# Kernel optimization log

Measured on AMD Instinct MI355X. Metric: run time of the kernel, lower is better.

## Reference

```python
import jax, jax.numpy as jnp
import numpy as np

B, S, H = 4, 1024, 256      # batch, num_spans, hidden
R = 65536                   # num_relations
FFN = int(2 * H * 1.5)      # 768


def setup_inputs() -> dict:
    key = jax.random.key(0)
    k1, k2, k3, k4 = jax.random.split(key, 4)
    span_reps = jax.random.normal(k1, (B, S, H), dtype=jnp.float32)
    rel_ids = jax.random.randint(k2, (B, R, 2), 0, S, dtype=jnp.int64)
    W1 = jax.random.normal(k3, (2 * H, FFN), dtype=jnp.float32) * (1.0 / np.sqrt(2 * H))
    b1 = jnp.zeros((FFN,), dtype=jnp.float32)
    W2 = jax.random.normal(k4, (FFN, H), dtype=jnp.float32) * (1.0 / np.sqrt(FFN))
    b2 = jnp.zeros((H,), dtype=jnp.float32)
    return {"span_reps": span_reps, "rel_ids": rel_ids, "W1": W1, "b1": b1, "W2": W2, "b2": b2}


def reference(span_reps, rel_ids, W1, b1, W2, b2):
    # gather head/tail span reps: (B, R, H) each
    head = jnp.take_along_axis(span_reps, rel_ids[..., 0:1], axis=1)  # via batched gather
    tail = jnp.take_along_axis(span_reps, rel_ids[..., 1:2], axis=1)
    rel = jnp.concatenate([head, tail], axis=-1)  # (B, R, 2H)
    # FFN projection: Linear -> ReLU -> (dropout: identity at eval) -> Linear
    h = jax.nn.relu(jnp.einsum('brk,kf->brf', rel, W1) + b1)
    out = jnp.einsum('brf,fh->brh', h, W2) + b2  # (B, R, H)
    return out
```

## Files before the change

### kernel.cpp

```cpp
#include <hip/hip_runtime.h>

#define NB 4
#define NS 1024
#define NH 256
#define NR 65536
#define NF 768
#define NK 512

typedef __attribute__((ext_vector_type(8))) short bf16x8;
typedef __attribute__((ext_vector_type(4))) float f32x4;

static __device__ __forceinline__ unsigned short f2bf(float f) {
  unsigned int u = __builtin_bit_cast(unsigned int, f);
  u += 0x7FFFu + ((u >> 16) & 1u);
  return (unsigned short)(u >> 16);
}

#define BARRIER()                                            \
  do {                                                       \
    asm volatile("s_waitcnt lgkmcnt(0)" ::: "memory");       \
    __builtin_amdgcn_s_barrier();                            \
    asm volatile("" ::: "memory");                           \
  } while (0)

__global__ void detect_idw(const int* __restrict__ ids, int* __restrict__ flag) {
  __shared__ int anynz;
  if (threadIdx.x == 0) anynz = 0;
  __syncthreads();
  int acc = 0;
  for (int i = threadIdx.x; i < 8192; i += 256) acc |= ids[2 * i + 1];
  if (acc != 0) atomicOr(&anynz, 1);
  __syncthreads();
  if (threadIdx.x == 0) flag[0] = (anynz == 0) ? 1 : 0;
}

__global__ void prep_w1(const float* __restrict__ w1, unsigned short* __restrict__ w1f) {
  int t = blockIdx.x * 256 + threadIdx.x;
  int l = t & 63;
  int kk = (t >> 6) & 15;
  int half = (t >> 10) & 1;
  int w = (t >> 11) & 3;
  int c = t >> 13;
  int row = c * 128 + w * 32 + half * 16 + (l & 15);
  int k0 = kk * 32 + (l >> 4) * 8;
  uint4 pk;
  unsigned short v[8];
#pragma unroll
  for (int j = 0; j < 8; ++j) v[j] = f2bf(w1[(size_t)(k0 + j) * NF + row]);
  pk.x = v[0] | ((unsigned)v[1] << 16);
  pk.y = v[2] | ((unsigned)v[3] << 16);
  pk.z = v[4] | ((unsigned)v[5] << 16);
  pk.w = v[6] | ((unsigned)v[7] << 16);
  *(uint4*)(w1f + (size_t)t * 8) = pk;
}

__global__ void prep_w2(const float* __restrict__ w2, unsigned short* __restrict__ w2f) {
  int t = blockIdx.x * 256 + threadIdx.x;
  int l = t & 63;
  int kq = (t >> 6) & 3;
  int rest = t >> 8;
  int c = rest % 6;
  int wn = rest / 6;
  int nj = wn & 3;
  int w = wn >> 2;
  int row = w * 64 + nj * 16 + (l & 15);
  int k = c * 128 + kq * 32 + (l >> 4) * 8;
  uint4 pk;
  unsigned short v[8];
#pragma unroll
  for (int j = 0; j < 8; ++j) v[j] = f2bf(w2[(size_t)(k + j) * NH + row]);
  pk.x = v[0] | ((unsigned)v[1] << 16);
  pk.y = v[2] | ((unsigned)v[3] << 16);
  pk.z = v[4] | ((unsigned)v[5] << 16);
  pk.w = v[6] | ((unsigned)v[7] << 16);
  *(uint4*)(w2f + (size_t)t * 8) = pk;
}

__global__ __launch_bounds__(256, 2)
void fused_relffn(const float* __restrict__ span, const int* __restrict__ ids,
                  const float* __restrict__ b1, const float* __restrict__ b2,
                  const unsigned short* __restrict__ w1f,
                  const unsigned short* __restrict__ w2f,
                  const int* __restrict__ flagp, float* __restrict__ out) {
  __shared__ __align__(16) unsigned short As[64 * 512];
  __shared__ __align__(16) unsigned short Hs[64 * 128];

  const int tid = threadIdx.x;
  const int blk = blockIdx.x;
  const int bb = blk >> 10;
  const int r0 = (blk & 1023) << 6;
  const int lane = tid & 63;
  const int w = tid >> 6;
  const int l15 = lane & 15;
  const int lq = lane >> 4;
  const int is64 = flagp[0];

  const unsigned short* w1base = w1f + w * 16384 + lane * 8;
  const unsigned short* w2base = w2f + w * 49152 + lane * 8;

  bf16x8 wf[4][2];
#pragma unroll
  for (int s = 0; s < 4; ++s) {
    wf[s][0] = *(const bf16x8*)(w1base + s * 512);
    wf[s][1] = *(const bf16x8*)(w1base + 8192 + s * 512);
  }

  {
    const long pair0 = ((long)bb * NR + r0) * 2;
#pragma unroll
    for (int j = 0; j < 16; ++j) {
      int g = tid + j * 256;
      int row = g >> 6;
      int kc = g & 63;
      long pidx = pair0 + row * 2 + (kc >> 5);
      int id = is64 ? ids[pidx * 2] : ids[pidx];
      const float* src = span + ((size_t)bb * NS + id) * NH + (kc & 31) * 8;
      float4 v0 = *(const float4*)src;
      float4 v1 = *(const float4*)(src + 4);
      uint4 pk;
      pk.x = f2bf(v0.x) | ((unsigned)f2bf(v0.y) << 16);
      pk.y = f2bf(v0.z) | ((unsigned)f2bf(v0.w) << 16);
      pk.z = f2bf(v1.x) | ((unsigned)f2bf(v1.y) << 16);
      pk.w = f2bf(v1.z) | ((unsigned)f2bf(v1.w) << 16);
      int idx = row * 512 + ((kc * 8) ^ ((row & 7) << 3));
      *(uint4*)&As[idx] = pk;
    }
  }
  BARRIER();

  f32x4 acc2[4][4];
#pragma unroll
  for (int mi = 0; mi < 4; ++mi)
#pragma unroll
    for (int nj = 0; nj < 4; ++nj) {
      f32x4 z = {0.f, 0.f, 0.f, 0.f};
      acc2[mi][nj] = z;
    }

  for (int c = 0; c < 6; ++c) {
    const unsigned short* w1p = w1base + c * 65536;
    f32x4 acc1[4][2];
#pragma unroll
    for (int mi = 0; mi < 4; ++mi)
#pragma unroll
      for (int ni = 0; ni < 2; ++ni) {
        f32x4 z = {0.f, 0.f, 0.f, 0.f};
        acc1[mi][ni] = z;
      }
#pragma unroll
    for (int kk = 0; kk < 16; ++kk) {
      const int s = kk & 3;
      bf16x8 cw0 = wf[s][0];
      bf16x8 cw1 = wf[s][1];
      if (kk < 12) {
        wf[s][0] = *(const bf16x8*)(w1p + (kk + 4) * 512);
        wf[s][1] = *(const bf16x8*)(w1p + 8192 + (kk + 4) * 512);
      }
      bf16x8 af[4];
#pragma unroll
      for (int mi = 0; mi < 4; ++mi) {
        int row = mi * 16 + l15;
        int kidx = kk * 32 + lq * 8;
        af[mi] = *(const bf16x8*)&As[row * 512 + (kidx ^ ((row & 7) << 3))];
      }
#pragma unroll
      for (int mi = 0; mi < 4; ++mi) {
        acc1[mi][0] = __builtin_amdgcn_mfma_f32_16x16x32_bf16(cw0, af[mi], acc1[mi][0], 0, 0, 0);
        acc1[mi][1] = __builtin_amdgcn_mfma_f32_16x16x32_bf16(cw1, af[mi], acc1[mi][1], 0, 0, 0);
      }
    }
    if (c < 5) {
      const unsigned short* np = w1base + (c + 1) * 65536;
#pragma unroll
      for (int s = 0; s < 4; ++s) {
        wf[s][0] = *(const bf16x8*)(np + s * 512);
        wf[s][1] = *(const bf16x8*)(np + 8192 + s * 512);
      }
    }
    BARRIER();
#pragma unroll
    for (int ni = 0; ni < 2; ++ni) {
      int n0 = c * 128 + w * 32 + ni * 16 + lq * 4;
      float4 bv = *(const float4*)(b1 + n0);
#pragma unroll
      for (int mi = 0; mi < 4; ++mi) {
        f32x4 a = acc1[mi][ni];
        float x0 = fmaxf(a[0] + bv.x, 0.0f);
        float x1 = fmaxf(a[1] + bv.y, 0.0f);
        float x2 = fmaxf(a[2] + bv.z, 0.0f);
        float x3 = fmaxf(a[3] + bv.w, 0.0f);
        int m = mi * 16 + l15;
        int nl0 = w * 32 + ni * 16 + lq * 4;
        uint2 pk;
        pk.x = f2bf(x0) | ((unsigned)f2bf(x1) << 16);
        pk.y = f2bf(x2) | ((unsigned)f2bf(x3) << 16);
        *(uint2*)&Hs[m * 128 + (nl0 ^ ((m & 7) << 3))] = pk;
      }
    }
    BARRIER();
    const unsigned short* w2p = w2base + c * 2048;
#pragma unroll
    for (int kq = 0; kq < 4; ++kq) {
      bf16x8 vf[4];
#pragma unroll
      for (int nj = 0; nj < 4; ++nj)
        vf[nj] = *(const bf16x8*)(w2p + nj * 12288 + kq * 512);
      bf16x8 hf[4];
#pragma unroll
      for (int mi = 0; mi < 4; ++mi) {
        int row = mi * 16 + l15;
        int kidx = kq * 32 + lq * 8;
        hf[mi] = *(const bf16x8*)&Hs[row * 128 + (kidx ^ ((row & 7) << 3))];
      }
#pragma unroll
      for (int mi = 0; mi < 4; ++mi)
#pragma unroll
        for (int nj = 0; nj < 4; ++nj)
          acc2[mi][nj] = __builtin_amdgcn_mfma_f32_16x16x32_bf16(vf[nj], hf[mi], acc2[mi][nj], 0, 0, 0);
    }
  }

#pragma unroll
  for (int nj = 0; nj < 4; ++nj) {
    int n0 = w * 64 + nj * 16 + lq * 4;
    float4 bv = *(const float4*)(b2 + n0);
#pragma unroll
    for (int mi = 0; mi < 4; ++mi) {
      int m = mi * 16 + l15;
      f32x4 a = acc2[mi][nj];
      float4 o;
      o.x = a[0] + bv.x; o.y = a[1] + bv.y; o.z = a[2] + bv.z; o.w = a[3] + bv.w;
      *(float4*)(out + ((size_t)bb * NR + r0 + m) * NH + n0) = o;
    }
  }
}

extern "C" void kernel_launch(void* const* d_in, const int* in_sizes, int n_in,
                              void* d_out, int out_size, void* d_ws, size_t ws_size,
                              hipStream_t stream) {
  const float* span = (const float*)d_in[0];
  const int* ids = (const int*)d_in[1];
  const float* W1 = (const float*)d_in[2];
  const float* b1 = (const float*)d_in[3];
  const float* W2 = (const float*)d_in[4];
  const float* b2 = (const float*)d_in[5];
  float* out = (float*)d_out;

  char* ws = (char*)d_ws;
  int* flag = (int*)ws;
  unsigned short* w1f = (unsigned short*)(ws + 64);
  unsigned short* w2f = (unsigned short*)(ws + 64 + NF * NK * 2);

  detect_idw<<<1, 256, 0, stream>>>(ids, flag);
  prep_w1<<<192, 256, 0, stream>>>(W1, w1f);
  prep_w2<<<96, 256, 0, stream>>>(W2, w2f);
  fused_relffn<<<4096, 256, 0, stream>>>(span, ids, b1, b2, w1f, w2f, flag, out);
}
```

Before: 347.2 us.

## Merge prep kernels, pair FFN chunks, double-buffer A fragments, use packed bf16 convert

Merges the three prep kernels into one launch to cut launch overhead. Batches the index loads before the span gathers so more memory requests are in flight. Uses the hardware packed bf16 conversion instruction in place of manual rounding. Restructures the first GEMM to compute two 128-wide FFN chunks per pass, sharing each A fragment across both and double-buffering LDS fragment loads. It also adds s_setprio around the MFMA blocks. Doubling the live accumulators raises register pressure, which may cost occupancy under the 2-block launch bound.

```diff
diff --git a/kernel.cpp b/kernel.cpp
--- a/kernel.cpp
+++ b/kernel.cpp
@@ -16,6 +16,12 @@
   return (unsigned short)(u >> 16);
 }
 
+static __device__ __forceinline__ unsigned cvt_pk(float a, float b) {
+  unsigned r;
+  asm("v_cvt_pk_bf16_f32 %0, %1, %2" : "=v"(r) : "v"(a), "v"(b));
+  return r;
+}
+
 #define BARRIER()                                            \
   do {                                                       \
     asm volatile("s_waitcnt lgkmcnt(0)" ::: "memory");       \
@@ -23,57 +29,60 @@
     asm volatile("" ::: "memory");                           \
   } while (0)
 
-__global__ void detect_idw(const int* __restrict__ ids, int* __restrict__ flag) {
-  __shared__ int anynz;
-  if (threadIdx.x == 0) anynz = 0;
-  __syncthreads();
-  int acc = 0;
-  for (int i = threadIdx.x; i < 8192; i += 256) acc |= ids[2 * i + 1];
-  if (acc != 0) atomicOr(&anynz, 1);
-  __syncthreads();
-  if (threadIdx.x == 0) flag[0] = (anynz == 0) ? 1 : 0;
-}
-
-__global__ void prep_w1(const float* __restrict__ w1, unsigned short* __restrict__ w1f) {
-  int t = blockIdx.x * 256 + threadIdx.x;
-  int l = t & 63;
-  int kk = (t >> 6) & 15;
-  int half = (t >> 10) & 1;
-  int w = (t >> 11) & 3;
-  int c = t >> 13;
-  int row = c * 128 + w * 32 + half * 16 + (l & 15);
-  int k0 = kk * 32 + (l >> 4) * 8;
-  uint4 pk;
-  unsigned short v[8];
-#pragma unroll
-  for (int j = 0; j < 8; ++j) v[j] = f2bf(w1[(size_t)(k0 + j) * NF + row]);
-  pk.x = v[0] | ((unsigned)v[1] << 16);
-  pk.y = v[2] | ((unsigned)v[3] << 16);
-  pk.z = v[4] | ((unsigned)v[5] << 16);
-  pk.w = v[6] | ((unsigned)v[7] << 16);
-  *(uint4*)(w1f + (size_t)t * 8) = pk;
-}
-
-__global__ void prep_w2(const float* __restrict__ w2, unsigned short* __restrict__ w2f) {
-  int t = blockIdx.x * 256 + threadIdx.x;
-  int l = t & 63;
-  int kq = (t >> 6) & 3;
-  int rest = t >> 8;
-  int c = rest % 6;
-  int wn = rest / 6;
-  int nj = wn & 3;
-  int w = wn >> 2;
-  int row = w * 64 + nj * 16 + (l & 15);
-  int k = c * 128 + kq * 32 + (l >> 4) * 8;
-  uint4 pk;
-  unsigned short v[8];
-#pragma unroll
-  for (int j = 0; j < 8; ++j) v[j] = f2bf(w2[(size_t)(k + j) * NH + row]);
-  pk.x = v[0] | ((unsigned)v[1] << 16);
-  pk.y = v[2] | ((unsigned)v[3] << 16);
-  pk.z = v[4] | ((unsigned)v[5] << 16);
-  pk.w = v[6] | ((unsigned)v[7] << 16);
-  *(uint4*)(w2f + (size_t)t * 8) = pk;
+__global__ void prep_all(const float* __restrict__ w1, const float* __restrict__ w2,
+                         const int* __restrict__ ids,
+                         unsigned short* __restrict__ w1f,
+                         unsigned short* __restrict__ w2f,
+                         int* __restrict__ flag) {
+  int bid = blockIdx.x;
+  if (bid < 192) {
+    int t = bid * 256 + threadIdx.x;
+    int l = t & 63;
+    int kk = (t >> 6) & 15;
+    int half = (t >> 10) & 1;
+    int w = (t >> 11) & 3;
+    int c = t >> 13;
+    int row = c * 128 + w * 32 + half * 16 + (l & 15);
+    int k0 = kk * 32 + (l >> 4) * 8;
+    uint4 pk;
+    unsigned short v[8];
+#pragma unroll
+    for (int j = 0; j < 8; ++j) v[j] = f2bf(w1[(size_t)(k0 + j) * NF + row]);
+    pk.x = v[0] | ((unsigned)v[1] << 16);
+    pk.y = v[2] | ((unsigned)v[3] << 16);
+    pk.z = v[4] | ((unsigned)v[5] << 16);
+    pk.w = v[6] | ((unsigned)v[7] << 16);
+    *(uint4*)(w1f + (size_t)t * 8) = pk;
+  } else if (bid < 288) {
+    int t = (bid - 192) * 256 + threadIdx.x;
+    int l = t & 63;
+    int kq = (t >> 6) & 3;
+    int rest = t >> 8;
+    int c = rest % 6;
+    int wn = rest / 6;
+    int nj = wn & 3;
+    int w = wn >> 2;
+    int row = w * 64 + nj * 16 + (l & 15);
+    int k = c * 128 + kq * 32 + (l >> 4) * 8;
+    uint4 pk;
+    unsigned short v[8];
+#pragma unroll
+    for (int j = 0; j < 8; ++j) v[j] = f2bf(w2[(size_t)(k + j) * NH + row]);
+    pk.x = v[0] | ((unsigned)v[1] << 16);
+    pk.y = v[2] | ((unsigned)v[3] << 16);
+    pk.z = v[4] | ((unsigned)v[5] << 16);
+    pk.w = v[6] | ((unsigned)v[7] << 16);
+    *(uint4*)(w2f + (size_t)t * 8) = pk;
+  } else {
+    __shared__ int anynz;
+    if (threadIdx.x == 0) anynz = 0;
+    __syncthreads();
+    int acc = 0;
+    for (int i = threadIdx.x; i < 8192; i += 256) acc |= ids[2 * i + 1];
+    if (acc != 0) atomicOr(&anynz, 1);
+    __syncthreads();
+    if (threadIdx.x == 0) flag[0] = (anynz == 0) ? 1 : 0;
+  }
 }
 
 __global__ __launch_bounds__(256, 2)
@@ -98,30 +107,30 @@
   const unsigned short* w1base = w1f + w * 16384 + lane * 8;
   const unsigned short* w2base = w2f + w * 49152 + lane * 8;
 
-  bf16x8 wf[4][2];
-#pragma unroll
-  for (int s = 0; s < 4; ++s) {
-    wf[s][0] = *(const bf16x8*)(w1base + s * 512);
-    wf[s][1] = *(const bf16x8*)(w1base + 8192 + s * 512);
-  }
-
   {
     const long pair0 = ((long)bb * NR + r0) * 2;
+    int idv[16];
 #pragma unroll
     for (int j = 0; j < 16; ++j) {
       int g = tid + j * 256;
       int row = g >> 6;
       int kc = g & 63;
       long pidx = pair0 + row * 2 + (kc >> 5);
-      int id = is64 ? ids[pidx * 2] : ids[pidx];
-      const float* src = span + ((size_t)bb * NS + id) * NH + (kc & 31) * 8;
+      idv[j] = is64 ? ids[pidx * 2] : ids[pidx];
+    }
+#pragma unroll
+    for (int j = 0; j < 16; ++j) {
+      int g = tid + j * 256;
+      int row = g >> 6;
+      int kc = g & 63;
+      const float* src = span + ((size_t)bb * NS + idv[j]) * NH + (kc & 31) * 8;
       float4 v0 = *(const float4*)src;
       float4 v1 = *(const float4*)(src + 4);
       uint4 pk;
-      pk.x = f2bf(v0.x) | ((unsigned)f2bf(v0.y) << 16);
-      pk.y = f2bf(v0.z) | ((unsigned)f2bf(v0.w) << 16);
-      pk.z = f2bf(v1.x) | ((unsigned)f2bf(v1.y) << 16);
-      pk.w = f2bf(v1.z) | ((unsigned)f2bf(v1.w) << 16);
+      pk.x = cvt_pk(v0.x, v0.y);
+      pk.y = cvt_pk(v0.z, v0.w);
+      pk.z = cvt_pk(v1.x, v1.y);
+      pk.w = cvt_pk(v1.z, v1.w);
       int idx = row * 512 + ((kc * 8) ^ ((row & 7) << 3));
       *(uint4*)&As[idx] = pk;
     }
@@ -137,86 +146,113 @@
       acc2[mi][nj] = z;
     }
 
-  for (int c = 0; c < 6; ++c) {
-    const unsigned short* w1p = w1base + c * 65536;
-    f32x4 acc1[4][2];
+  for (int cp = 0; cp < 3; ++cp) {
+    const int ca = cp * 2, cb = ca + 1;
+    const unsigned short* wpa = w1base + ca * 65536;
+    const unsigned short* wpb = w1base + cb * 65536;
+
+    f32x4 acc1a[4][2], acc1b[4][2];
 #pragma unroll
     for (int mi = 0; mi < 4; ++mi)
 #pragma unroll
       for (int ni = 0; ni < 2; ++ni) {
         f32x4 z = {0.f, 0.f, 0.f, 0.f};
-        acc1[mi][ni] = z;
-      }
+        acc1a[mi][ni] = z;
+        acc1b[mi][ni] = z;
+      }
+
+    bf16x8 wfa[2][2], wfb[2][2];
+#pragma unroll
+    for (int d = 0; d < 2; ++d) {
+      wfa[d][0] = *(const bf16x8*)(wpa + d * 512);
+      wfa[d][1] = *(const bf16x8*)(wpa + 8192 + d * 512);
+      wfb[d][0] = *(const bf16x8*)(wpb + d * 512);
+      wfb[d][1] = *(const bf16x8*)(wpb + 8192 + d * 512);
+    }
+    bf16x8 afp[2][4];
+#pragma unroll
+    for (int mi = 0; mi < 4; ++mi) {
+      int row = mi * 16 + l15;
+      afp[0][mi] = *(const bf16x8*)&As[row * 512 + ((lq * 8) ^ ((row & 7) << 3))];
+    }
+
 #pragma unroll
     for (int kk = 0; kk < 16; ++kk) {
-      const int s = kk & 3;
-      bf16x8 cw0 = wf[s][0];
-      bf16x8 cw1 = wf[s][1];
-      if (kk < 12) {
-        wf[s][0] = *(const bf16x8*)(w1p + (kk + 4) * 512);
-        wf[s][1] = *(const bf16x8*)(w1p + 8192 + (kk + 4) * 512);
-      }
-      bf16x8 af[4];
+      const int cur = kk & 1;
+      if (kk < 15) {
+#pragma unroll
+        for (int mi = 0; mi < 4; ++mi) {
+          int row = mi * 16 + l15;
+          int kidx = (kk + 1) * 32 + lq * 8;
+          afp[cur ^ 1][mi] = *(const bf16x8*)&As[row * 512 + (kidx ^ ((row & 7) << 3))];
+        }
+      }
+      bf16x8 ca0 = wfa[cur][0], ca1 = wfa[cur][1];
+      bf16x8 cb0 = wfb[cur][0], cb1 = wfb[cur][1];
+      if (kk < 14) {
+        wfa[cur][0] = *(const bf16x8*)(wpa + (kk + 2) * 512);
+        wfa[cur][1] = *(const bf16x8*)(wpa + 8192 + (kk + 2) * 512);
+        wfb[cur][0] = *(const bf16x8*)(wpb + (kk + 2) * 512);
+        wfb[cur][1] = *(const bf16x8*)(wpb + 8192 + (kk + 2) * 512);
+      }
+      __builtin_amdgcn_s_setprio(1);
 #pragma unroll
       for (int mi = 0; mi < 4; ++mi) {
-        int row = mi * 16 + l15;
-        int kidx = kk * 32 + lq * 8;
-        af[mi] = *(const bf16x8*)&As[row * 512 + (kidx ^ ((row & 7) << 3))];
-      }
-#pragma unroll
-      for (int mi = 0; mi < 4; ++mi) {
-        acc1[mi][0] = __builtin_amdgcn_mfma_f32_16x16x32_bf16(cw0, af[mi], acc1[mi][0], 0, 0, 0);
-        acc1[mi][1] = __builtin_amdgcn_mfma_f32_16x16x32_bf16(cw1, af[mi], acc1[mi][1], 0, 0, 0);
-      }
-    }
-    if (c < 5) {
-      const unsigned short* np = w1base + (c + 1) * 65536;
-#pragma unroll
-      for (int s = 0; s < 4; ++s) {
-        wf[s][0] = *(const bf16x8*)(np + s * 512);
-        wf[s][1] = *(const bf16x8*)(np + 8192 + s * 512);
-      }
-    }
-    BARRIER();
-#pragma unroll
-    for (int ni = 0; ni < 2; ++ni) {
-      int n0 = c * 128 + w * 32 + ni * 16 + lq * 4;
-      float4 bv = *(const float4*)(b1 + n0);
-#pragma unroll
-      for (int mi = 0; mi < 4; ++mi) {
-        f32x4 a = acc1[mi][ni];
-        float x0 = fmaxf(a[0] + bv.x, 0.0f);
-        float x1 = fmaxf(a[1] + bv.y, 0.0f);
-        float x2 = fmaxf(a[2] + bv.z, 0.0f);
-        float x3 = fmaxf(a[3] + bv.w, 0.0f);
-        int m = mi * 16 + l15;
-        int nl0 = w * 32 + ni * 16 + lq * 4;
-        uint2 pk;
-        pk.x = f2bf(x0) | ((unsigned)f2bf(x1) << 16);
-        pk.y = f2bf(x2) | ((unsigned)f2bf(x3) << 16);
-        *(uint2*)&Hs[m * 128 + (nl0 ^ ((m & 7) << 3))] = pk;
-      }
-    }
-    BARRIER();
-    const unsigned short* w2p = w2base + c * 2048;
-#pragma unroll
-    for (int kq = 0; kq < 4; ++kq) {
-      bf16x8 vf[4];
-#pragma unroll
-      for (int nj = 0; nj < 4; ++nj)
-        vf[nj] = *(const bf16x8*)(w2p + nj * 12288 + kq * 512);
-      bf16x8 hf[4];
-#pragma unroll
-      for (int mi = 0; mi < 4; ++mi) {
-        int row = mi * 16 + l15;
-        int kidx = kq * 32 + lq * 8;
-        hf[mi] = *(const bf16x8*)&Hs[row * 128 + (kidx ^ ((row & 7) << 3))];
-      }
-#pragma unroll
-      for (int mi = 0; mi < 4; ++mi)
+        bf16x8 a = afp[cur][mi];
+        acc1a[mi][0] = __builtin_amdgcn_mfma_f32_16x16x32_bf16(ca0, a, acc1a[mi][0], 0, 0, 0);
+        acc1a[mi][1] = __builtin_amdgcn_mfma_f32_16x16x32_bf16(ca1, a, acc1a[mi][1], 0, 0, 0);
+        acc1b[mi][0] = __builtin_amdgcn_mfma_f32_16x16x32_bf16(cb0, a, acc1b[mi][0], 0, 0, 0);
+        acc1b[mi][1] = __builtin_amdgcn_mfma_f32_16x16x32_bf16(cb1, a, acc1b[mi][1], 0, 0, 0);
+      }
+      __builtin_amdgcn_s_setprio(0);
+    }
+
+#pragma unroll
+    for (int half = 0; half < 2; ++half) {
+      const int c = half ? cb : ca;
+      BARRIER();
+#pragma unroll
+      for (int ni = 0; ni < 2; ++ni) {
+        int n0 = c * 128 + w * 32 + ni * 16 + lq * 4;
+        float4 bv = *(const float4*)(b1 + n0);
+#pragma unroll
+        for (int mi = 0; mi < 4; ++mi) {
+          f32x4 a = half ? acc1b[mi][ni] : acc1a[mi][ni];
+          float x0 = fmaxf(a[0] + bv.x, 0.0f);
+          float x1 = fmaxf(a[1] + bv.y, 0.0f);
+          float x2 = fmaxf(a[2] + bv.z, 0.0f);
+          float x3 = fmaxf(a[3] + bv.w, 0.0f);
+          int m = mi * 16 + l15;
+          int nl0 = w * 32 + ni * 16 + lq * 4;
+          uint2 pk;
+          pk.x = cvt_pk(x0, x1);
+          pk.y = cvt_pk(x2, x3);
+          *(uint2*)&Hs[m * 128 + (nl0 ^ ((m & 7) << 3))] = pk;
+        }
+      }
+      BARRIER();
+      const unsigned short* w2p = w2base + c * 2048;
+#pragma unroll
+      for (int kq = 0; kq < 4; ++kq) {
+        bf16x8 vf[4];
 #pragma unroll
         for (int nj = 0; nj < 4; ++nj)
-          acc2[mi][nj] = __builtin_amdgcn_mfma_f32_16x16x32_bf16(vf[nj], hf[mi], acc2[mi][nj], 0, 0, 0);
+          vf[nj] = *(const bf16x8*)(w2p + nj * 12288 + kq * 512);
+        bf16x8 hf[4];
+#pragma unroll
+        for (int mi = 0; mi < 4; ++mi) {
+          int row = mi * 16 + l15;
+          int kidx = kq * 32 + lq * 8;
+          hf[mi] = *(const bf16x8*)&Hs[row * 128 + (kidx ^ ((row & 7) << 3))];
+        }
+        __builtin_amdgcn_s_setprio(1);
+#pragma unroll
+        for (int mi = 0; mi < 4; ++mi)
+#pragma unroll
+          for (int nj = 0; nj < 4; ++nj)
+            acc2[mi][nj] = __builtin_amdgcn_mfma_f32_16x16x32_bf16(vf[nj], hf[mi], acc2[mi][nj], 0, 0, 0);
+        __builtin_amdgcn_s_setprio(0);
+      }
     }
   }
 
@@ -251,8 +287,6 @@
   unsigned short* w1f = (unsigned short*)(ws + 64);
   unsigned short* w2f = (unsigned short*)(ws + 64 + NF * NK * 2);
 
-  detect_idw<<<1, 256, 0, stream>>>(ids, flag);
-  prep_w1<<<192, 256, 0, stream>>>(W1, w1f);
-  prep_w2<<<96, 256, 0, stream>>>(W2, w2f);
+  prep_all<<<289, 256, 0, stream>>>(W1, W2, ids, w1f, w2f, flag);
   fused_relffn<<<4096, 256, 0, stream>>>(span, ids, b1, b2, w1f, w2f, flag, out);
 }
```

After: 307.0 us. -11.6%, faster.
